# Performance work log

Measured on AMD Instinct MI355X. Metric: run time of the kernel, lower is better.

Reference implementation:

```python
import jax, jax.numpy as jnp
import numpy as np

N_SRC, M, K, H = 100000, 20000, 32, 128
NEG_SLOPE = 0.01  # torch LeakyReLU default


def setup_inputs() -> dict:
    key = jax.random.key(0)
    ks = jax.random.split(key, 8)
    nei = jax.random.randint(ks[0], (M, K), 0, N_SRC)
    h = jax.random.normal(ks[1], (N_SRC, 1), dtype=jnp.float32)
    h_refer = jax.random.normal(ks[2], (M, 1), dtype=jnp.float32)
    # map_l / map_r: Linear(1, H), weight init U[0,1), bias U[0,0.01)
    map_l_w = jax.random.uniform(ks[3], (H, 1), dtype=jnp.float32)
    map_l_b = jax.random.uniform(ks[4], (H,), dtype=jnp.float32) * 0.01
    map_r_w = jax.random.uniform(ks[5], (H, 1), dtype=jnp.float32)
    map_r_b = jax.random.uniform(ks[6], (H,), dtype=jnp.float32) * 0.01
    # att_inter: xavier_normal gain=1.414 on shape (1, 2H)
    std = 1.414 * np.sqrt(2.0 / (1 + 2 * H))
    att_inter = jax.random.normal(ks[7], (1, 2 * H), dtype=jnp.float32) * std
    return {"nei": nei, "h": h, "h_refer": h_refer,
            "map_l_w": map_l_w, "map_l_b": map_l_b,
            "map_r_w": map_r_w, "map_r_b": map_r_b,
            "att_inter": att_inter}


def reference(nei, h, h_refer, map_l_w, map_l_b, map_r_w, map_r_b, att_inter):
    # project scalar features to H dims
    h = jax.nn.relu(h @ map_l_w.T + map_l_b)            # [N, H]
    hr = jax.nn.relu(h_refer @ map_r_w.T + map_r_b)     # [M, H]
    nei_emb = h[nei]                                    # [M, K, H] gather
    # split attention vector to avoid materializing concat([hr, nei_emb])
    a_ref = att_inter[0, :H]                            # [H]
    a_nei = att_inter[0, H:]                            # [H]
    logits = (hr @ a_ref)[:, None] + nei_emb @ a_nei    # [M, K]
    logits = jnp.where(logits >= 0, logits, NEG_SLOPE * logits)  # leakyrelu
    att = jax.nn.softmax(logits, axis=1)                # softmax over neighbors
    lr_inner = jnp.einsum('mkh,mh->mk', nei_emb, hr)    # [M, K]
    out = jax.nn.relu(jnp.sum(att * lr_inner, axis=1, keepdims=True))  # [M, 1]
    return (out, att)
```

## Files before the change

kernel.cpp:

```cpp
#include <hip/hip_runtime.h>

#define N_SRC 100000
#define M_NODES 20000
#define K_NEI 32
#define H_DIM 128
#define NEG_SLOPE 0.01f

__global__ __launch_bounds__(256) void intra_att_kernel(
    const int*   __restrict__ nei,
    const float* __restrict__ h,
    const float* __restrict__ h_refer,
    const float* __restrict__ map_l_w,
    const float* __restrict__ map_l_b,
    const float* __restrict__ map_r_w,
    const float* __restrict__ map_r_b,
    const float* __restrict__ att_inter,
    float*       __restrict__ out,
    float*       __restrict__ att)
{
    __shared__ float s_wl[H_DIM];
    __shared__ float s_bl[H_DIM];
    __shared__ float s_an[H_DIM];
    __shared__ float s_hr[8][H_DIM];

    const int tid = threadIdx.x;

    if (tid < H_DIM) {
        s_wl[tid] = map_l_w[tid];
        s_bl[tid] = map_l_b[tid];
        s_an[tid] = att_inter[H_DIM + tid];
    }

    const int wave  = tid >> 6;
    const int lane  = tid & 63;
    const int half  = lane >> 5;
    const int l32   = lane & 31;
    const int mslot = wave * 2 + half;
    const int m     = blockIdx.x * 8 + mslot;
    const bool valid = (m < M_NODES);

    __syncthreads();

    float hrdot = 0.f;
    {
        const float hrefm = valid ? h_refer[m] : 0.f;
        const int j = l32 * 4;
        const float4 wr4 = *(const float4*)(map_r_w + j);
        const float4 br4 = *(const float4*)(map_r_b + j);
        const float4 ar4 = *(const float4*)(att_inter + j);
        float4 hr4;
        hr4.x = fmaxf(0.f, fmaf(hrefm, wr4.x, br4.x));
        hr4.y = fmaxf(0.f, fmaf(hrefm, wr4.y, br4.y));
        hr4.z = fmaxf(0.f, fmaf(hrefm, wr4.z, br4.z));
        hr4.w = fmaxf(0.f, fmaf(hrefm, wr4.w, br4.w));
        *(float4*)(&s_hr[mslot][j]) = hr4;
        hrdot = hr4.x*ar4.x + hr4.y*ar4.y + hr4.z*ar4.z + hr4.w*ar4.w;
        #pragma unroll
        for (int o = 16; o >= 1; o >>= 1) hrdot += __shfl_xor(hrdot, o);
    }
    __syncthreads();

    float logit = 0.f;
    float inner = 0.f;
    if (valid) {
        const int   idx = nei[m * K_NEI + l32];
        const float h_i = h[idx];
        const float* hrp = s_hr[mslot];
        #pragma unroll 8
        for (int j = 0; j < H_DIM; j += 4) {
            const float4 wl4 = *(const float4*)(s_wl + j);
            const float4 bl4 = *(const float4*)(s_bl + j);
            const float4 an4 = *(const float4*)(s_an + j);
            const float4 hr4 = *(const float4*)(hrp + j);
            const float e0 = fmaxf(0.f, fmaf(h_i, wl4.x, bl4.x));
            const float e1 = fmaxf(0.f, fmaf(h_i, wl4.y, bl4.y));
            const float e2 = fmaxf(0.f, fmaf(h_i, wl4.z, bl4.z));
            const float e3 = fmaxf(0.f, fmaf(h_i, wl4.w, bl4.w));
            logit = fmaf(e0, an4.x, logit);
            logit = fmaf(e1, an4.y, logit);
            logit = fmaf(e2, an4.z, logit);
            logit = fmaf(e3, an4.w, logit);
            inner = fmaf(e0, hr4.x, inner);
            inner = fmaf(e1, hr4.y, inner);
            inner = fmaf(e2, hr4.z, inner);
            inner = fmaf(e3, hr4.w, inner);
        }
    }
    logit += hrdot;
    logit = (logit >= 0.f) ? logit : NEG_SLOPE * logit;

    float wmax = logit;
    #pragma unroll
    for (int o = 16; o >= 1; o >>= 1) wmax = fmaxf(wmax, __shfl_xor(wmax, o));
    const float e = expf(logit - wmax);
    float se  = e;
    float sei = e * inner;
    #pragma unroll
    for (int o = 16; o >= 1; o >>= 1) {
        se  += __shfl_xor(se,  o);
        sei += __shfl_xor(sei, o);
    }

    if (valid) {
        att[m * K_NEI + l32] = e / se;
        if (l32 == 0) out[m] = fmaxf(0.f, sei / se);
    }
}

extern "C" void kernel_launch(void* const* d_in, const int* in_sizes, int n_in,
                              void* d_out, int out_size, void* d_ws, size_t ws_size,
                              hipStream_t stream) {
    const int*   nei       = (const int*)  d_in[0];
    const float* h         = (const float*)d_in[1];
    const float* h_refer   = (const float*)d_in[2];
    const float* map_l_w   = (const float*)d_in[3];
    const float* map_l_b   = (const float*)d_in[4];
    const float* map_r_w   = (const float*)d_in[5];
    const float* map_r_b   = (const float*)d_in[6];
    const float* att_inter = (const float*)d_in[7];

    float* out = (float*)d_out;
    float* att = out + M_NODES;

    const int blocks = (M_NODES + 7) / 8;
    intra_att_kernel<<<blocks, 256, 0, stream>>>(
        nei, h, h_refer, map_l_w, map_l_b, map_r_w, map_r_b, att_inter,
        out, att);
}
```

Baseline: 20.36 us.

## Process four neighbors per thread with 32 nodes per block and vectorized I/O

```diff
diff --git a/kernel.cpp b/kernel.cpp
--- a/kernel.cpp
+++ b/kernel.cpp
@@ -5,6 +5,9 @@
 #define K_NEI 32
 #define H_DIM 128
 #define NEG_SLOPE 0.01f
+
+#define BLK_M 32
+#define HR_PAD 132
 
 __global__ __launch_bounds__(256) void intra_att_kernel(
     const int*   __restrict__ nei,
@@ -18,12 +21,19 @@
     float*       __restrict__ out,
     float*       __restrict__ att)
 {
-    __shared__ float s_wl[H_DIM];
-    __shared__ float s_bl[H_DIM];
-    __shared__ float s_an[H_DIM];
-    __shared__ float s_hr[8][H_DIM];
+    __shared__ __attribute__((aligned(16))) float s_wl[H_DIM];
+    __shared__ __attribute__((aligned(16))) float s_bl[H_DIM];
+    __shared__ __attribute__((aligned(16))) float s_an[H_DIM];
+    __shared__ __attribute__((aligned(16))) float s_hr[BLK_M][HR_PAD];
 
-    const int tid = threadIdx.x;
+    const int tid  = threadIdx.x;
+    const int slot = tid >> 3;
+    const int sub  = tid & 7;
+    const int m    = blockIdx.x * BLK_M + slot;
+
+    const int4 nv = *(const int4*)(nei + m * K_NEI + sub * 4);
+    float h_i[4];
+    h_i[0] = h[nv.x]; h_i[1] = h[nv.y]; h_i[2] = h[nv.z]; h_i[3] = h[nv.w];
 
     if (tid < H_DIM) {
         s_wl[tid] = map_l_w[tid];
@@ -31,80 +41,81 @@
         s_an[tid] = att_inter[H_DIM + tid];
     }
 
-    const int wave  = tid >> 6;
-    const int lane  = tid & 63;
-    const int half  = lane >> 5;
-    const int l32   = lane & 31;
-    const int mslot = wave * 2 + half;
-    const int m     = blockIdx.x * 8 + mslot;
-    const bool valid = (m < M_NODES);
-
-    __syncthreads();
-
+    const float rm = h_refer[m];
     float hrdot = 0.f;
     {
-        const float hrefm = valid ? h_refer[m] : 0.f;
-        const int j = l32 * 4;
-        const float4 wr4 = *(const float4*)(map_r_w + j);
-        const float4 br4 = *(const float4*)(map_r_b + j);
-        const float4 ar4 = *(const float4*)(att_inter + j);
-        float4 hr4;
-        hr4.x = fmaxf(0.f, fmaf(hrefm, wr4.x, br4.x));
-        hr4.y = fmaxf(0.f, fmaf(hrefm, wr4.y, br4.y));
-        hr4.z = fmaxf(0.f, fmaf(hrefm, wr4.z, br4.z));
-        hr4.w = fmaxf(0.f, fmaf(hrefm, wr4.w, br4.w));
-        *(float4*)(&s_hr[mslot][j]) = hr4;
-        hrdot = hr4.x*ar4.x + hr4.y*ar4.y + hr4.z*ar4.z + hr4.w*ar4.w;
+        const int jb = sub * 16;
         #pragma unroll
-        for (int o = 16; o >= 1; o >>= 1) hrdot += __shfl_xor(hrdot, o);
+        for (int c = 0; c < 16; c += 4) {
+            const float4 wr4 = *(const float4*)(map_r_w + jb + c);
+            const float4 br4 = *(const float4*)(map_r_b + jb + c);
+            const float4 ar4 = *(const float4*)(att_inter + jb + c);
+            float4 hr4;
+            hr4.x = fmaxf(0.f, fmaf(rm, wr4.x, br4.x));
+            hr4.y = fmaxf(0.f, fmaf(rm, wr4.y, br4.y));
+            hr4.z = fmaxf(0.f, fmaf(rm, wr4.z, br4.z));
+            hr4.w = fmaxf(0.f, fmaf(rm, wr4.w, br4.w));
+            *(float4*)(&s_hr[slot][jb + c]) = hr4;
+            hrdot += hr4.x*ar4.x + hr4.y*ar4.y + hr4.z*ar4.z + hr4.w*ar4.w;
+        }
+        #pragma unroll
+        for (int o = 4; o >= 1; o >>= 1) hrdot += __shfl_xor(hrdot, o);
     }
     __syncthreads();
 
-    float logit = 0.f;
-    float inner = 0.f;
-    if (valid) {
-        const int   idx = nei[m * K_NEI + l32];
-        const float h_i = h[idx];
-        const float* hrp = s_hr[mslot];
-        #pragma unroll 8
-        for (int j = 0; j < H_DIM; j += 4) {
-            const float4 wl4 = *(const float4*)(s_wl + j);
-            const float4 bl4 = *(const float4*)(s_bl + j);
-            const float4 an4 = *(const float4*)(s_an + j);
-            const float4 hr4 = *(const float4*)(hrp + j);
-            const float e0 = fmaxf(0.f, fmaf(h_i, wl4.x, bl4.x));
-            const float e1 = fmaxf(0.f, fmaf(h_i, wl4.y, bl4.y));
-            const float e2 = fmaxf(0.f, fmaf(h_i, wl4.z, bl4.z));
-            const float e3 = fmaxf(0.f, fmaf(h_i, wl4.w, bl4.w));
-            logit = fmaf(e0, an4.x, logit);
-            logit = fmaf(e1, an4.y, logit);
-            logit = fmaf(e2, an4.z, logit);
-            logit = fmaf(e3, an4.w, logit);
-            inner = fmaf(e0, hr4.x, inner);
-            inner = fmaf(e1, hr4.y, inner);
-            inner = fmaf(e2, hr4.z, inner);
-            inner = fmaf(e3, hr4.w, inner);
+    float lg[4] = {0.f, 0.f, 0.f, 0.f};
+    float in_[4] = {0.f, 0.f, 0.f, 0.f};
+    const float* hrp = s_hr[slot];
+    #pragma unroll 8
+    for (int j = 0; j < H_DIM; j += 4) {
+        const float4 wl4 = *(const float4*)(s_wl + j);
+        const float4 bl4 = *(const float4*)(s_bl + j);
+        const float4 an4 = *(const float4*)(s_an + j);
+        const float4 hr4 = *(const float4*)(hrp + j);
+        #pragma unroll
+        for (int t = 0; t < 4; ++t) {
+            const float hi = h_i[t];
+            const float e0 = fmaxf(0.f, fmaf(hi, wl4.x, bl4.x));
+            const float e1 = fmaxf(0.f, fmaf(hi, wl4.y, bl4.y));
+            const float e2 = fmaxf(0.f, fmaf(hi, wl4.z, bl4.z));
+            const float e3 = fmaxf(0.f, fmaf(hi, wl4.w, bl4.w));
+            lg[t] = fmaf(e0, an4.x, lg[t]);
+            lg[t] = fmaf(e1, an4.y, lg[t]);
+            lg[t] = fmaf(e2, an4.z, lg[t]);
+            lg[t] = fmaf(e3, an4.w, lg[t]);
+            in_[t] = fmaf(e0, hr4.x, in_[t]);
+            in_[t] = fmaf(e1, hr4.y, in_[t]);
+            in_[t] = fmaf(e2, hr4.z, in_[t]);
+            in_[t] = fmaf(e3, hr4.w, in_[t]);
         }
     }
-    logit += hrdot;
-    logit = (logit >= 0.f) ? logit : NEG_SLOPE * logit;
 
-    float wmax = logit;
     #pragma unroll
-    for (int o = 16; o >= 1; o >>= 1) wmax = fmaxf(wmax, __shfl_xor(wmax, o));
-    const float e = expf(logit - wmax);
-    float se  = e;
-    float sei = e * inner;
+    for (int t = 0; t < 4; ++t) {
+        float l = lg[t] + hrdot;
+        lg[t] = (l >= 0.f) ? l : NEG_SLOPE * l;
+    }
+
+    float mx = fmaxf(fmaxf(lg[0], lg[1]), fmaxf(lg[2], lg[3]));
     #pragma unroll
-    for (int o = 16; o >= 1; o >>= 1) {
+    for (int o = 4; o >= 1; o >>= 1) mx = fmaxf(mx, __shfl_xor(mx, o));
+
+    float e[4];
+    #pragma unroll
+    for (int t = 0; t < 4; ++t) e[t] = __expf(lg[t] - mx);
+    float se  = e[0] + e[1] + e[2] + e[3];
+    float sei = e[0]*in_[0] + e[1]*in_[1] + e[2]*in_[2] + e[3]*in_[3];
+    #pragma unroll
+    for (int o = 4; o >= 1; o >>= 1) {
         se  += __shfl_xor(se,  o);
         sei += __shfl_xor(sei, o);
     }
 
-    if (valid) {
-        att[m * K_NEI + l32] = e / se;
-        if (l32 == 0) out[m] = fmaxf(0.f, sei / se);
-    }
+    const float inv = 1.0f / se;
+    float4 a4;
+    a4.x = e[0] * inv; a4.y = e[1] * inv; a4.z = e[2] * inv; a4.w = e[3] * inv;
+    *(float4*)(att + m * K_NEI + sub * 4) = a4;
+    if (sub == 0) out[m] = fmaxf(0.f, sei * inv);
 }
 
 extern "C" void kernel_launch(void* const* d_in, const int* in_sizes, int n_in,
@@ -122,7 +133,7 @@
     float* out = (float*)d_out;
     float* att = out + M_NODES;
 
-    const int blocks = (M_NODES + 7) / 8;
+    const int blocks = M_NODES / BLK_M;
     intra_att_kernel<<<blocks, 256, 0, stream>>>(
         nei, h, h_refer, map_l_w, map_l_b, map_r_w, map_r_b, att_inter,
         out, att);
```

Result: faster. 19.03 us (-6.5%).
